# Performance work log

Measured on AMD Instinct MI355X. Metric: run time of the kernel, lower is better.

The kernel has to match this reference:

```python
import jax, jax.numpy as jnp
import numpy as np

D_MODEL = 1024
D_STATE = 16
EXPAND = 2
D_HEAD = 64
D_CONV = 4
FFN = 2816
NORMALIZE_BC = True
D_INNER = EXPAND * D_MODEL          # 2048
N_HEADS = D_INNER // D_HEAD         # 32
EPS = 1e-6


def _rmsnorm(x, w):
    v = jnp.mean(x * x, axis=-1, keepdims=True)
    return x * jax.lax.rsqrt(v + EPS) * w


def _mixer(x, in_proj_w, conv_w, conv_b, A_log, dt_bias, D, out_proj_w):
    b, l, _ = x.shape
    zxbcdt = x @ in_proj_w.T  # (b, l, 2*D_INNER + 2*D_STATE + N_HEADS)
    z, xBC, dt_raw = jnp.split(zxbcdt, [D_INNER, 2 * D_INNER + 2 * D_STATE], axis=-1)
    # causal depthwise conv over (u, B, C) channels
    xp = jnp.pad(xBC, ((0, 0), (D_CONV - 1, 0), (0, 0)))
    y = conv_b + sum(xp[:, k:k + l, :] * conv_w[:, k] for k in range(D_CONV))
    xBC = jax.nn.silu(y)
    u, Bm, Cm = jnp.split(xBC, [D_INNER, D_INNER + D_STATE], axis=-1)
    if NORMALIZE_BC:
        Bm = Bm / (jnp.linalg.norm(Bm, axis=-1, keepdims=True) + EPS)
        Cm = Cm / (jnp.linalg.norm(Cm, axis=-1, keepdims=True) + EPS)
    dt = jax.nn.softplus(dt_raw + dt_bias)          # (b, l, h)
    A = jnp.exp(A_log)                              # (h, n) oscillator frequencies >= 0
    u = u.reshape(b, l, N_HEADS, D_HEAD)

    # LinOSS implicit (IM) discretization of z' = -A y + B u ; y' = z
    #   S  = 1/(1 + dt^2 A)
    #   w_k = S*(w_{k-1} - dt*A*y_{k-1} + dt*B u_k)
    #   y_k = y_{k-1} + dt*w_k ;  out_k = C y_k + D u_k
    def step(carry, inp):
        w, ys = carry                               # each (b, h, dh, n)
        dt_t, B_t, C_t, u_t = inp                   # (b,h),(b,n),(b,n),(b,h,dh)
        S = 1.0 / (1.0 + (dt_t[:, :, None] ** 2) * A[None])   # (b,h,n)
        Sb = S[:, :, None, :]
        dtb = dt_t[:, :, None, None]
        Ab = A[None, :, None, :]
        Bu = B_t[:, None, None, :] * u_t[..., None]            # (b,h,dh,n)
        w = Sb * (w - dtb * Ab * ys + dtb * Bu)
        ys = ys + dtb * w
        o = jnp.einsum('bhdn,bn->bhd', ys, C_t)
        return (w, ys), o

    init = (jnp.zeros((b, N_HEADS, D_HEAD, D_STATE), x.dtype),
            jnp.zeros((b, N_HEADS, D_HEAD, D_STATE), x.dtype))
    xs = (dt.transpose(1, 0, 2), Bm.transpose(1, 0, 2),
          Cm.transpose(1, 0, 2), u.transpose(1, 0, 2, 3))
    _, ys = jax.lax.scan(step, init, xs)            # (l, b, h, dh)
    ys = ys.transpose(1, 0, 2, 3) + D[None, None, :, None] * u
    out = ys.reshape(b, l, D_INNER) * jax.nn.silu(z)
    return out @ out_proj_w.T


def setup_inputs() -> dict:
    key = jax.random.key(0)
    ks = jax.random.split(key, 12)
    B, L = 4, 2048
    proj_dim = 2 * D_INNER + 2 * D_STATE + N_HEADS
    conv_ch = D_INNER + 2 * D_STATE
    s = lambda k, shape, sc: jax.random.normal(k, shape, jnp.float32) * sc
    return {
        "x": s(ks[0], (B, L, D_MODEL), 1.0),
        "norm1_w": jnp.ones((D_MODEL,), jnp.float32),
        "in_proj_w": s(ks[1], (proj_dim, D_MODEL), D_MODEL ** -0.5),
        "conv_w": s(ks[2], (conv_ch, D_CONV), 0.3),
        "conv_b": jnp.zeros((conv_ch,), jnp.float32),
        "A_log": s(ks[3], (N_HEADS, D_STATE), 0.5),
        "dt_bias": s(ks[4], (N_HEADS,), 0.5),
        "D": s(ks[5], (N_HEADS,), 1.0),
        "out_proj_w": s(ks[6], (D_MODEL, D_INNER), D_INNER ** -0.5),
        "norm2_w": jnp.ones((D_MODEL,), jnp.float32),
        "gate_w": s(ks[7], (FFN, D_MODEL), D_MODEL ** -0.5),
        "up_w": s(ks[8], (FFN, D_MODEL), D_MODEL ** -0.5),
        "down_w": s(ks[9], (D_MODEL, FFN), FFN ** -0.5),
    }


def reference(x, norm1_w, in_proj_w, conv_w, conv_b, A_log, dt_bias, D,
              out_proj_w, norm2_w, gate_w, up_w, down_w):
    h = x + _mixer(_rmsnorm(x, norm1_w), in_proj_w, conv_w, conv_b,
                   A_log, dt_bias, D, out_proj_w)
    hn = _rmsnorm(h, norm2_w)
    ffn = (jax.nn.silu(hn @ gate_w.T) * (hn @ up_w.T)) @ down_w.T
    return h + ffn
```

## Files before the change

### kernel.cpp

```cpp
#include <hip/hip_runtime.h>
#include <hip/hip_bf16.h>

#define D_MODEL   1024
#define D_STATE   16
#define D_HEAD    64
#define D_CONV    4
#define FFN_DIM   2816
#define D_INNER   2048
#define N_HEADS   32
#define BATCH     4
#define SEQ       2048
#define ROWS      (BATCH*SEQ)
#define PROJ_DIM  4160
#define PROJ_PAD  4352
#define CONV_CH   2080
#define CH        128
#define NCH       (SEQ/CH)
#define GU_N      5632

typedef __bf16 bf16x8 __attribute__((ext_vector_type(8)));
typedef float  f32x4  __attribute__((ext_vector_type(4)));
typedef float  f32x2  __attribute__((ext_vector_type(2)));

__device__ __forceinline__ float siluf(float x) { return x / (1.0f + __expf(-x)); }

#define SBAR() do { asm volatile("" ::: "memory"); __builtin_amdgcn_s_barrier(); asm volatile("" ::: "memory"); } while (0)
#define LGKM0() asm volatile("s_waitcnt lgkmcnt(0)" ::: "memory")
#define VMCNT4() asm volatile("s_waitcnt vmcnt(4)" ::: "memory")
#define VMCNT2() asm volatile("s_waitcnt vmcnt(2)" ::: "memory")
#define VMCNT0() asm volatile("s_waitcnt vmcnt(0)" ::: "memory")

__global__ void cvt_k(const float* __restrict__ src, __hip_bfloat16* __restrict__ dst, int n) {
  int i = blockIdx.x * blockDim.x + threadIdx.x;
  if (i < n) dst[i] = __float2bfloat16(src[i]);
}

__global__ void cvt_pad_k(const float* __restrict__ src, __hip_bfloat16* __restrict__ dst) {
  int i = blockIdx.x * blockDim.x + threadIdx.x;
  if (i >= PROJ_PAD * D_MODEL) return;
  int row = i >> 10;
  dst[i] = (row < PROJ_DIM) ? __float2bfloat16(src[i]) : __float2bfloat16(0.0f);
}

__global__ void cvt_gu_k(const float* __restrict__ wg, const float* __restrict__ wu,
                         __hip_bfloat16* __restrict__ dst) {
  int i = blockIdx.x * blockDim.x + threadIdx.x;
  if (i >= GU_N * D_MODEL) return;
  int r = i >> 10, c = i & 1023;
  int tile = r >> 8, rr = r & 255;
  const float* src = (rr < 128)
      ? wg + (size_t)(tile * 128 + rr) * D_MODEL + c
      : wu + (size_t)(tile * 128 + (rr - 128)) * D_MODEL + c;
  dst[i] = __float2bfloat16(*src);
}

__global__ __launch_bounds__(256) void rmsnorm_k(const float* __restrict__ x,
                                                 const float* __restrict__ w,
                                                 __hip_bfloat16* __restrict__ out,
                                                 float* __restrict__ outf) {
  int row = blockIdx.x;
  int t = threadIdx.x;
  const float* xr = x + (size_t)row * D_MODEL;
  float4 v = ((const float4*)xr)[t];
  float ss = v.x*v.x + v.y*v.y + v.z*v.z + v.w*v.w;
  #pragma unroll
  for (int o = 32; o > 0; o >>= 1) ss += __shfl_xor(ss, o);
  __shared__ float red[4];
  if ((t & 63) == 0) red[t >> 6] = ss;
  __syncthreads();
  ss = red[0] + red[1] + red[2] + red[3];
  float scale = rsqrtf(ss * (1.0f / D_MODEL) + 1e-6f);
  float4 wv = ((const float4*)w)[t];
  float4 r;
  r.x = v.x * scale * wv.x; r.y = v.y * scale * wv.y;
  r.z = v.z * scale * wv.z; r.w = v.w * scale * wv.w;
  __hip_bfloat16* orow = out + (size_t)row * D_MODEL + t * 4;
  orow[0] = __float2bfloat16(r.x);
  orow[1] = __float2bfloat16(r.y);
  orow[2] = __float2bfloat16(r.z);
  orow[3] = __float2bfloat16(r.w);
  if (outf) ((float4*)(outf + (size_t)row * D_MODEL))[t] = r;
}

__global__ __launch_bounds__(256) void dtproj_k(const float* __restrict__ xn,
                                                const float* __restrict__ wi,
                                                const float* __restrict__ dtb,
                                                float* __restrict__ dtT) {
  const int r0 = blockIdx.x * 4;
  const int t  = threadIdx.x;
  const int hh  = t >> 3;
  const int seg = t & 7;

  __shared__ float xs[4][D_MODEL];
  #pragma unroll
  for (int i = 0; i < 4; ++i)
    ((float4*)&xs[i][0])[t] = ((const float4*)(xn + (size_t)(r0 + i) * D_MODEL))[t];
  __syncthreads();

  const float4* w4 = (const float4*)(wi + (size_t)(2 * D_INNER + 2 * D_STATE + hh) * D_MODEL) + seg * 32;
  const float4* x0 = (const float4*)&xs[0][0] + seg * 32;
  const float4* x1 = (const float4*)&xs[1][0] + seg * 32;
  const float4* x2 = (const float4*)&xs[2][0] + seg * 32;
  const float4* x3 = (const float4*)&xs[3][0] + seg * 32;
  float a0 = 0.f, a1 = 0.f, a2 = 0.f, a3 = 0.f;
  #pragma unroll 8
  for (int k = 0; k < 32; ++k) {
    float4 wv = w4[k];
    float4 v0 = x0[k], v1 = x1[k], v2 = x2[k], v3 = x3[k];
    a0 = fmaf(wv.x, v0.x, fmaf(wv.y, v0.y, fmaf(wv.z, v0.z, fmaf(wv.w, v0.w, a0))));
    a1 = fmaf(wv.x, v1.x, fmaf(wv.y, v1.y, fmaf(wv.z, v1.z, fmaf(wv.w, v1.w, a1))));
    a2 = fmaf(wv.x, v2.x, fmaf(wv.y, v2.y, fmaf(wv.z, v2.z, fmaf(wv.w, v2.w, a2))));
    a3 = fmaf(wv.x, v3.x, fmaf(wv.y, v3.y, fmaf(wv.z, v3.z, fmaf(wv.w, v3.w, a3))));
  }
  #pragma unroll
  for (int m = 1; m < 8; m <<= 1) {
    a0 += __shfl_xor(a0, m);
    a1 += __shfl_xor(a1, m);
    a2 += __shfl_xor(a2, m);
    a3 += __shfl_xor(a3, m);
  }
  if (seg == 0) {
    float bias = dtb[hh];
    float v[4] = {a0, a1, a2, a3};
    #pragma unroll
    for (int i = 0; i < 4; ++i) {
      float xv = v[i] + bias;
      dtT[(size_t)hh * ROWS + r0 + i] = (xv > 20.f) ? xv : log1pf(__expf(xv));
    }
  }
}

template<int EPI>
__global__ __launch_bounds__(512, 2) void gemm8(
    const __hip_bfloat16* __restrict__ A,
    const __hip_bfloat16* __restrict__ Bw,
    float* __restrict__ Cf,
    __hip_bfloat16* __restrict__ Cb,
    const float* __restrict__ add_src,
    int M, int N, int K)
{
  extern __shared__ char lds[];
  const int nwg = (M >> 8) * (N >> 8);
  int bid = blockIdx.x;
  bid = (bid & 7) * (nwg >> 3) + (bid >> 3);
  const int ntn = N >> 8;
  const int bm = (bid / ntn) << 8;
  const int bn = (bid % ntn) << 8;

  const int tid  = threadIdx.x;
  const int wid  = tid >> 6;
  const int lane = tid & 63;
  const int wm = wid >> 2;
  const int wn = wid & 3;
  const int r16 = lane & 15;
  const int kg  = lane >> 4;

  const int rb = ((r16 << 6) + (kg << 4)) ^ ((r16 & 8) << 2);

  const int s_sub = tid >> 6;
  const int s_w   = (tid & 63) << 4;
  const int s_wp  = s_w ^ ((((s_w) >> 9) & 1) << 5);
  const int s_row = ((s_sub >> 1) << 4) + (s_wp >> 6);
  const int s_col = ((s_sub & 1) << 5) + ((s_wp >> 1) & 31);

  auto stage = [&](int buf, int mat, int half, int c, int kt) {
    const __hip_bfloat16* src = (mat == 0)
        ? A  + (size_t)(bm + half * 128 + c * 64 + s_row) * K + kt * 64 + s_col
        : Bw + (size_t)(bn + half * 128 + c * 64 + s_row) * K + kt * 64 + s_col;
    char* dst = lds + buf * 65536 + mat * 32768 + half * 16384 + c * 8192 + tid * 16;
    __builtin_amdgcn_global_load_lds((const __attribute__((address_space(1))) unsigned int*)src,
                                     (__attribute__((address_space(3))) unsigned int*)dst,
                                     16, 0, 0);
  };

  f32x4 acc[8][4] = {};
  bf16x8 af[4][2], bfr[4][2];

  const int NT = K >> 6;
  stage(0,0,0,0,0); stage(0,0,0,1,0); stage(0,0,1,0,0); stage(0,0,1,1,0);
  stage(0,1,0,0,0); stage(0,1,0,1,0); stage(0,1,1,0,0); stage(0,1,1,1,0);
  __syncthreads();

  for (int kt = 0; kt < NT; ++kt) {
    const int buf = kt & 1, nbuf = buf ^ 1;
    const bool st = (kt + 1 < NT);
    const char* Ab = lds + buf * 65536 + wm * 16384;
    const char* Bb = lds + buf * 65536 + 32768 + (wn >> 1) * 16384 + (wn & 1) * 8192;

    #pragma unroll
    for (int mi2 = 0; mi2 < 4; ++mi2)
      #pragma unroll
      for (int kk = 0; kk < 2; ++kk)
        af[mi2][kk] = *(const bf16x8*)(Ab + (mi2 * 2 + kk) * 1024 + rb);
    #pragma unroll
    for (int ni = 0; ni < 2; ++ni)
      #pragma unroll
      for (int kk = 0; kk < 2; ++kk)
        bfr[ni][kk] = *(const bf16x8*)(Bb + (ni * 2 + kk) * 1024 + rb);
    if (st) { stage(nbuf,1,0,0,kt+1); stage(nbuf,1,0,1,kt+1); }
    SBAR(); LGKM0();
    __builtin_amdgcn_s_setprio(1);
    #pragma unroll
    for (int mi2 = 0; mi2 < 4; ++mi2)
      #pragma unroll
      for (int ni = 0; ni < 2; ++ni)
        #pragma unroll
        for (int kk = 0; kk < 2; ++kk)
          acc[mi2][ni] = __builtin_amdgcn_mfma_f32_16x16x32_bf16(af[mi2][kk], bfr[ni][kk], acc[mi2][ni], 0, 0, 0);
    __builtin_amdgcn_s_setprio(0);
    SBAR();

    #pragma unroll
    for (int ni = 2; ni < 4; ++ni)
      #pragma unroll
      for (int kk = 0; kk < 2; ++kk)
        bfr[ni][kk] = *(const bf16x8*)(Bb + (ni * 2 + kk) * 1024 + rb);
    if (st) { stage(nbuf,1,1,0,kt+1); stage(nbuf,1,1,1,kt+1); }
    SBAR(); LGKM0();
    __builtin_amdgcn_s_setprio(1);
    #pragma unroll
    for (int mi2 = 0; mi2 < 4; ++mi2)
      #pragma unroll
      for (int ni = 2; ni < 4; ++ni)
        #pragma unroll
        for (int kk = 0; kk < 2; ++kk)
          acc[mi2][ni] = __builtin_amdgcn_mfma_f32_16x16x32_bf16(af[mi2][kk], bfr[ni][kk], acc[mi2][ni], 0, 0, 0);
    __builtin_amdgcn_s_setprio(0);
    if (st) { VMCNT4(); } else { VMCNT0(); }
    SBAR();

    #pragma unroll
    for (int mi2 = 0; mi2 < 4; ++mi2)
      #pragma unroll
      for (int kk = 0; kk < 2; ++kk)
        af[mi2][kk] = *(const bf16x8*)(Ab + ((4 + mi2) * 2 + kk) * 1024 + rb);
    if (st) { stage(nbuf,0,0,0,kt+1); stage(nbuf,0,1,0,kt+1); }
    SBAR(); LGKM0();
    __builtin_amdgcn_s_setprio(1);
    #pragma unroll
    for (int mi2 = 0; mi2 < 4; ++mi2)
      #pragma unroll
      for (int ni = 0; ni < 2; ++ni)
        #pragma unroll
        for (int kk = 0; kk < 2; ++kk)
          acc[4 + mi2][ni] = __builtin_amdgcn_mfma_f32_16x16x32_bf16(af[mi2][kk], bfr[ni][kk], acc[4 + mi2][ni], 0, 0, 0);
    __builtin_amdgcn_s_setprio(0);
    SBAR();

    if (st) { stage(nbuf,0,0,1,kt+1); stage(nbuf,0,1,1,kt+1); }
    SBAR(); LGKM0();
    __builtin_amdgcn_s_setprio(1);
    #pragma unroll
    for (int mi2 = 0; mi2 < 4; ++mi2)
      #pragma unroll
      for (int ni = 2; ni < 4; ++ni)
        #pragma unroll
        for (int kk = 0; kk < 2; ++kk)
          acc[4 + mi2][ni] = __builtin_amdgcn_mfma_f32_16x16x32_bf16(af[mi2][kk], bfr[ni][kk], acc[4 + mi2][ni], 0, 0, 0);
    __builtin_amdgcn_s_setprio(0);
    VMCNT2();
    SBAR();
  }

  if constexpr (EPI == 4) {
    float* xch = (float*)lds;
    __syncthreads();
    if (wn < 2) {
      #pragma unroll
      for (int mi = 0; mi < 8; ++mi)
        #pragma unroll
        for (int ni = 0; ni < 4; ++ni)
          #pragma unroll
          for (int j = 0; j < 4; ++j) {
            int row = mi * 16 + kg * 4 + j;
            int col = wn * 64 + ni * 16 + r16;
            int cc = col ^ (((row >> 2) & 1) << 4);
            xch[wm * 16384 + row * 128 + cc] = siluf(acc[mi][ni][j]);
          }
    }
    __syncthreads();
    if (wn >= 2) {
      #pragma unroll
      for (int mi = 0; mi < 8; ++mi)
        #pragma unroll
        for (int ni = 0; ni < 4; ++ni)
          #pragma unroll
          for (int j = 0; j < 4; ++j) {
            int row = mi * 16 + kg * 4 + j;
            int col = (wn - 2) * 64 + ni * 16 + r16;
            int cc = col ^ (((row >> 2) & 1) << 4);
            float g = xch[wm * 16384 + row * 128 + cc];
            int r = bm + wm * 128 + row;
            int tc = (bn >> 1) + col;
            Cb[(size_t)r * FFN_DIM + tc] = __float2bfloat16(g * acc[mi][ni][j]);
          }
    }
  } else {
    #pragma unroll
    for (int mi = 0; mi < 8; ++mi) {
      #pragma unroll
      for (int ni = 0; ni < 4; ++ni) {
        #pragma unroll
        for (int j = 0; j < 4; ++j) {
          int r = bm + wm * 128 + mi * 16 + kg * 4 + j;
          int c = bn + wn * 64 + ni * 16 + r16;
          size_t idx = (size_t)r * N + c;
          float v = acc[mi][ni][j];
          if constexpr (EPI == 0) {
            Cf[idx] = v;
          } else if constexpr (EPI == 1) {
            Cf[idx] = v + add_src[idx];
          }
        }
      }
    }
  }
}

template<int EPI>
__global__ __launch_bounds__(512, 2) void gemm8B(
    const __hip_bfloat16* __restrict__ A,
    const __hip_bfloat16* __restrict__ Bw,
    float* __restrict__ Cf,
    __hip_bfloat16* __restrict__ Cb,
    const float* __restrict__ add_src,
    int M, int N, int K)
{
  extern __shared__ char lds[];
  const int nwg = (M >> 8) * (N >> 7);
  int bid = blockIdx.x;
  bid = (bid & 7) * (nwg >> 3) + (bid >> 3);
  const int ntn = N >> 7;
  const int bm = (bid / ntn) << 8;
  const int bn = (bid % ntn) << 7;

  const int tid  = threadIdx.x;
  const int wid  = tid >> 6;
  const int lane = tid & 63;
  const int wm = wid >> 2;
  const int wn = wid & 3;
  const int r16 = lane & 15;
  const int kg  = lane >> 4;

  const int rb = ((r16 << 6) + (kg << 4)) ^ ((r16 & 8) << 2);

  const int s_sub = tid >> 6;
  const int s_w   = (tid & 63) << 4;
  const int s_wp  = s_w ^ ((((s_w) >> 9) & 1) << 5);
  const int s_row = ((s_sub >> 1) << 4) + (s_wp >> 6);
  const int s_col = ((s_sub & 1) << 5) + ((s_wp >> 1) & 31);

  auto stageA = [&](int buf, int half, int c, int kt) {
    const __hip_bfloat16* src = A + (size_t)(bm + half * 128 + c * 64 + s_row) * K + kt * 64 + s_col;
    char* dst = lds + buf * 65536 + half * 16384 + c * 8192 + tid * 16;
    __builtin_amdgcn_global_load_lds((const __attribute__((address_space(1))) unsigned int*)src,
                                     (__attribute__((address_space(3))) unsigned int*)dst,
                                     16, 0, 0);
  };
  auto stageB = [&](int buf, int c, int kt) {
    const __hip_bfloat16* src = Bw + (size_t)(bn + c * 64 + s_row) * K + kt * 64 + s_col;
    char* dst = lds + buf * 65536 + 32768 + c * 8192 + tid * 16;
    __builtin_amdgcn_global_load_lds((const __attribute__((address_space(1))) unsigned int*)src,
                                     (__attribute__((address_space(3))) unsigned int*)dst,
                                     16, 0, 0);
  };

  f32x4 acc[8][2] = {};
  bf16x8 af[4][2], bfr[2][2];

  const int NT = K >> 6;
  stageB(0,0,0); stageB(0,1,0);
  stageA(0,0,0,0); stageA(0,1,0,0); stageA(0,0,1,0); stageA(0,1,1,0);
  __syncthreads();

  for (int kt = 0; kt < NT; ++kt) {
    const int buf = kt & 1, nbuf = buf ^ 1;
    const bool st = (kt + 1 < NT);
    const char* Ab = lds + buf * 65536 + wm * 16384;
    const char* Bb = lds + buf * 65536 + 32768 + (wn >> 1) * 8192 + (wn & 1) * 4096;

    #pragma unroll
    for (int mi2 = 0; mi2 < 4; ++mi2)
      #pragma unroll
      for (int kk = 0; kk < 2; ++kk)
        af[mi2][kk] = *(const bf16x8*)(Ab + (mi2 * 2 + kk) * 1024 + rb);
    #pragma unroll
    for (int ni = 0; ni < 2; ++ni)
      #pragma unroll
      for (int kk = 0; kk < 2; ++kk)
        bfr[ni][kk] = *(const bf16x8*)(Bb + (ni * 2 + kk) * 1024 + rb);
    if (st) { stageB(nbuf,0,kt+1); stageB(nbuf,1,kt+1); stageA(nbuf,0,0,kt+1); stageA(nbuf,1,0,kt+1); }
    SBAR(); LGKM0();
    __builtin_amdgcn_s_setprio(1);
    #pragma unroll
    for (int mi2 = 0; mi2 < 4; ++mi2)
      #pragma unroll
      for (int ni = 0; ni < 2; ++ni)
        #pragma unroll
        for (int kk = 0; kk < 2; ++kk)
          acc[mi2][ni] = __builtin_amdgcn_mfma_f32_16x16x32_bf16(af[mi2][kk], bfr[ni][kk], acc[mi2][ni], 0, 0, 0);
    __builtin_amdgcn_s_setprio(0);
    if (st) { VMCNT4(); } else { VMCNT0(); }
    SBAR();

    #pragma unroll
    for (int mi2 = 0; mi2 < 4; ++mi2)
      #pragma unroll
      for (int kk = 0; kk < 2; ++kk)
        af[mi2][kk] = *(const bf16x8*)(Ab + ((4 + mi2) * 2 + kk) * 1024 + rb);
    if (st) { stageA(nbuf,0,1,kt+1); stageA(nbuf,1,1,kt+1); }
    SBAR(); LGKM0();
    __builtin_amdgcn_s_setprio(1);
    #pragma unroll
    for (int mi2 = 0; mi2 < 4; ++mi2)
      #pragma unroll
      for (int ni = 0; ni < 2; ++ni)
        #pragma unroll
        for (int kk = 0; kk < 2; ++kk)
          acc[4 + mi2][ni] = __builtin_amdgcn_mfma_f32_16x16x32_bf16(af[mi2][kk], bfr[ni][kk], acc[4 + mi2][ni], 0, 0, 0);
    __builtin_amdgcn_s_setprio(0);
    VMCNT2();
    SBAR();
  }

  #pragma unroll
  for (int mi = 0; mi < 8; ++mi) {
    #pragma unroll
    for (int ni = 0; ni < 2; ++ni) {
      #pragma unroll
      for (int j = 0; j < 4; ++j) {
        int r = bm + wm * 128 + mi * 16 + kg * 4 + j;
        int c = bn + wn * 32 + ni * 16 + r16;
        size_t idx = (size_t)r * N + c;
        float v = acc[mi][ni][j];
        if constexpr (EPI == 0) {
          Cf[idx] = v;
        } else if constexpr (EPI == 1) {
          Cf[idx] = v + add_src[idx];
        }
      }
    }
  }
}

__global__ __launch_bounds__(256) void duconv_k(const float* __restrict__ zx,
                                                const float* __restrict__ cw,
                                                const float* __restrict__ cb,
                                                __hip_bfloat16* __restrict__ u_po) {
  int idx = blockIdx.x * 256 + threadIdx.x;
  int q = idx & 511;
  int r = idx >> 9;
  int d0 = q << 2;
  int l = r & (SEQ - 1);
  float4 cb4 = ((const float4*)cb)[q];
  float tw[4][4];
  #pragma unroll
  for (int i = 0; i < 4; ++i) {
    float4 t = ((const float4*)cw)[d0 + i];
    tw[i][0] = t.x; tw[i][1] = t.y; tw[i][2] = t.z; tw[i][3] = t.w;
  }
  float a[4] = {cb4.x, cb4.y, cb4.z, cb4.w};
  #pragma unroll
  for (int k = 0; k < 4; ++k) {
    if (l - 3 + k >= 0) {
      float4 xv = *(const float4*)(zx + (size_t)(r - 3 + k) * PROJ_PAD + D_INNER + d0);
      a[0] = fmaf(xv.x, tw[0][k], a[0]);
      a[1] = fmaf(xv.y, tw[1][k], a[1]);
      a[2] = fmaf(xv.z, tw[2][k], a[2]);
      a[3] = fmaf(xv.w, tw[3][k], a[3]);
    }
  }
  union { ushort4 u4; __hip_bfloat16 b[4]; } pk;
  #pragma unroll
  for (int i = 0; i < 4; ++i) pk.b[i] = __float2bfloat16(siluf(a[i]));
  *(ushort4*)(u_po + (size_t)r * D_INNER + d0) = pk.u4;
}

__global__ __launch_bounds__(256) void bcdt_k(const float* __restrict__ zx,
                                              const float* __restrict__ cw,
                                              const float* __restrict__ cb,
                                              float* __restrict__ bc) {
  int t = threadIdx.x;
  int r = blockIdx.x * 8 + (t >> 5);
  int ch = t & 31;
  int l = r & (SEQ - 1);
  int c = D_INNER + ch;
  float acc = cb[c];
  #pragma unroll
  for (int k = 0; k < 4; ++k) {
    int lp = l - 3 + k;
    if (lp >= 0)
      acc = fmaf(zx[(size_t)(r - 3 + k) * PROJ_PAD + 2 * D_INNER + ch], cw[c * 4 + k], acc);
  }
  acc = siluf(acc);
  float ss = acc * acc;
  ss += __shfl_xor(ss, 1);
  ss += __shfl_xor(ss, 2);
  ss += __shfl_xor(ss, 4);
  ss += __shfl_xor(ss, 8);
  bc[r * 32 + ch] = acc / (sqrtf(ss) + 1e-6f);
}

__global__ __launch_bounds__(256) void pk_k(const float* __restrict__ dtT,
                                            const float* __restrict__ A_log,
                                            float* __restrict__ Pm) {
  int bh = blockIdx.x;
  int h = bh & 31;
  int t = threadIdx.x;
  int ch = t >> 4, n = t & 15;
  float a = __expf(A_log[h * 16 + n]);
  const float* dtp = dtT + (size_t)h * ROWS + (size_t)(bh >> 5) * SEQ + ch * CH;
  float p00 = 1.f, p01 = 0.f, p10 = 0.f, p11 = 1.f;
  for (int l = 0; l < CH; ++l) {
    float dt = dtp[l];
    float s  = 1.0f / fmaf(dt * dt, a, 1.0f);
    float m00 = s;
    float m01 = -dt * a * s;
    float m10 = dt * s;
    float m11 = fmaf(-dt * a, m10, 1.0f);
    float q00 = fmaf(m00, p00, m01 * p10);
    float q01 = fmaf(m00, p01, m01 * p11);
    float q10 = fmaf(m10, p00, m11 * p10);
    float q11 = fmaf(m10, p01, m11 * p11);
    p00 = q00; p01 = q01; p10 = q10; p11 = q11;
  }
  float4 v = {p00, p01, p10, p11};
  *(float4*)&Pm[(((size_t)bh * NCH + ch) * 16 + n) * 4] = v;
}

__global__ __launch_bounds__(256) void prop_k(const float* __restrict__ Pm,
                                              const float* __restrict__ pend,
                                              float* __restrict__ sinit) {
  int gid = blockIdx.x * 256 + threadIdx.x;
  int n  = gid & 15;
  int d  = (gid >> 4) & 63;
  int bh = gid >> 10;
  float s0 = 0.f, s1 = 0.f;
  for (int c = 0; c < NCH; ++c) {
    size_t i2 = (((size_t)bh * NCH + c) * 64 + d) * 16 + n;
    *(float2*)&sinit[i2 * 2] = make_float2(s0, s1);
    float4 P  = *(const float4*)&Pm[(((size_t)bh * NCH + c) * 16 + n) * 4];
    float2 pe = *(const float2*)&pend[i2 * 2];
    float t0 = fmaf(P.x, s0, fmaf(P.y, s1, pe.x));
    float t1 = fmaf(P.z, s0, fmaf(P.w, s1, pe.y));
    s0 = t0; s1 = t1;
  }
}

#define T_TILE 16
#define TPC (CH / T_TILE)
template<int PHASE>
__global__ __launch_bounds__(128) void scan_k(
    const float* __restrict__ zx, const float* __restrict__ bcb,
    const float* __restrict__ dtT, const float* __restrict__ A_log,
    const float* __restrict__ Dp, float* __restrict__ states,
    __hip_bfloat16* u_po)
{
  const int blk  = blockIdx.x;
  const int half = blk & 1;
  const int ch   = (blk >> 1) & 15;
  const int h    = (blk >> 5) & 31;
  const int b    = blk >> 10;
  const int bh   = b * 32 + h;
  const int tid  = threadIdx.x;
  const int wv   = tid >> 6;
  const int lane = tid & 63;
  const int d16  = lane & 15;
  const int ng   = lane >> 4;
  const int n0   = ng * 4;
  const int dwv  = wv * 16 + d16;
  const int dl   = half * 32 + dwv;
  const int dbase = h * 64 + half * 32;
  const size_t rowbase = (size_t)b * SEQ + (size_t)ch * CH;

  __shared__ __hip_bfloat16 dut[2][T_TILE][32];
  __shared__ float Btl[2][T_TILE][16];
  __shared__ float Ctl[PHASE == 3 ? 2 : 1][T_TILE][16];
  __shared__ float zt [PHASE == 3 ? 2 : 1][T_TILE][32];
  __shared__ float st [2][T_TILE][16];
  __shared__ float dtt[2][T_TILE];
  __shared__ float aexp[16];
  __shared__ float opart[PHASE == 3 ? T_TILE : 1][32][4];

  if (tid < 16) aexp[tid] = __expf(A_log[h * 16 + tid]);

  f32x2 A2[2];
  #pragma unroll
  for (int k = 0; k < 2; ++k) {
    A2[k][0] = __expf(A_log[h * 16 + n0 + 2 * k]);
    A2[k][1] = __expf(A_log[h * 16 + n0 + 2 * k + 1]);
  }
  const float Dh = Dp[h];

  auto stage = [&](int tile, int buf) {
    const size_t r0 = rowbase + (size_t)tile * T_TILE;
    if constexpr (PHASE == 3) {
      {
        int row = wv * 8 + (lane >> 3);
        const float* g = zx + (r0 + row) * PROJ_PAD + dbase + (lane & 7) * 4;
        float* l_ = &zt[buf][0][0] + wv * 256 + lane * 4;
        __builtin_amdgcn_global_load_lds((const __attribute__((address_space(1))) unsigned int*)g,
                                         (__attribute__((address_space(3))) unsigned int*)l_, 16, 0, 0);
      }
      if (wv == 0) {
        const __hip_bfloat16* g = u_po + (r0 + (lane >> 2)) * D_INNER + dbase + (lane & 3) * 8;
        __hip_bfloat16* l_ = &dut[buf][0][0] + lane * 8;
        __builtin_amdgcn_global_load_lds((const __attribute__((address_space(1))) unsigned int*)g,
                                         (__attribute__((address_space(3))) unsigned int*)l_, 16, 0, 0);
      } else {
        const float* gB = bcb + (r0 + (lane >> 2)) * 32 + (lane & 3) * 4;
        float* lB = &Btl[buf][0][0] + lane * 4;
        __builtin_amdgcn_global_load_lds((const __attribute__((address_space(1))) unsigned int*)gB,
                                         (__attribute__((address_space(3))) unsigned int*)lB, 16, 0, 0);
        const float* gC = bcb + (r0 + (lane >> 2)) * 32 + 16 + (lane & 3) * 4;
        float* lC = &Ctl[buf][0][0] + lane * 4;
        __builtin_amdgcn_global_load_lds((const __attribute__((address_space(1))) unsigned int*)gC,
                                         (__attribute__((address_space(3))) unsigned int*)lC, 16, 0, 0);
      }
    } else {
      if (wv == 0) {
        const __hip_bfloat16* g = u_po + (r0 + (lane >> 2)) * D_INNER + dbase + (lane & 3) * 8;
        __hip_bfloat16* l_ = &dut[buf][0][0] + lane * 8;
        __builtin_amdgcn_global_load_lds((const __attribute__((address_space(1))) unsigned int*)g,
                                         (__attribute__((address_space(3))) unsigned int*)l_, 16, 0, 0);
      } else {
        const float* gB = bcb + (r0 + (lane >> 2)) * 32 + (lane & 3) * 4;
        float* lB = &Btl[buf][0][0] + lane * 4;
        __builtin_amdgcn_global_load_lds((const __attribute__((address_space(1))) unsigned int*)gB,
                                         (__attribute__((address_space(3))) unsigned int*)lB, 16, 0, 0);
      }
    }
  };

  auto sprep = [&](int buf, float dtn) {
    #pragma unroll
    for (int i = 0; i < 2; ++i) {
      int idx = tid + 128 * i;
      int row = idx >> 4, n = idx & 15;
      float dv = __shfl(dtn, row);
      float a  = aexp[n];
      st[buf][row][n] = 1.0f / fmaf(dv * dv, a, 1.0f);
    }
  };

  stage(0, 0);
  float dtn = 0.f;
  if (lane < 16) dtn = dtT[(size_t)h * ROWS + rowbase + lane];
  __syncthreads();
  if (tid < 16) dtt[0][tid] = dtn;
  sprep(0, dtn);
  __syncthreads();

  f32x2 w2[2], ys2[2];
  if constexpr (PHASE == 1) {
    #pragma unroll
    for (int k = 0; k < 2; ++k) { w2[k] = (f32x2){0.f, 0.f}; ys2[k] = (f32x2){0.f, 0.f}; }
  } else {
    #pragma unroll
    for (int k = 0; k < 2; ++k)
      #pragma unroll
      for (int j = 0; j < 2; ++j) {
        size_t i2 = (((size_t)bh * NCH + ch) * 64 + dl) * 16 + (n0 + 2 * k + j);
        float2 s = *(const float2*)&states[i2 * 2];
        w2[k][j] = s.x; ys2[k][j] = s.y;
      }
  }
  int cur = 0;

  for (int t = 0; t < TPC; ++t) {
    if (t + 1 < TPC) {
      stage(t + 1, cur ^ 1);
      if (lane < 16) dtn = dtT[(size_t)h * ROWS + rowbase + (size_t)(t + 1) * T_TILE + lane];
    }
    #pragma unroll 4
    for (int l = 0; l < T_TILE; ++l) {
      float uv  = __bfloat162float(dut[cur][l][dwv]);
      float dtv = dtt[cur][l];
      f32x4 Sv4 = *(const f32x4*)&st [cur][l][n0];
      f32x4 Bv4 = *(const f32x4*)&Btl[cur][l][n0];
      float du = dtv * uv;
      f32x2 S2[2] = { {Sv4[0], Sv4[1]}, {Sv4[2], Sv4[3]} };
      f32x2 B2[2] = { {Bv4[0], Bv4[1]}, {Bv4[2], Bv4[3]} };
      if constexpr (PHASE == 3) {
        f32x4 Cv4 = *(const f32x4*)&Ctl[cur][l][n0];
        f32x2 C2[2] = { {Cv4[0], Cv4[1]}, {Cv4[2], Cv4[3]} };
        f32x2 o2 = {0.f, 0.f};
        #pragma unroll
        for (int k = 0; k < 2; ++k) {
          f32x2 dtA = dtv * A2[k];
          f32x2 tmp = w2[k] - dtA * ys2[k];
          tmp = tmp + du * B2[k];
          w2[k] = S2[k] * tmp;
          ys2[k] = ys2[k] + dtv * w2[k];
          o2 = o2 + ys2[k] * C2[k];
        }
        float o = o2[0] + o2[1];
        float ofin = (ng == 0) ? fmaf(Dh, uv, o) : o;
        opart[l][dwv][ng] = ofin;
      } else {
        #pragma unroll
        for (int k = 0; k < 2; ++k) {
          f32x2 dtA = dtv * A2[k];
          f32x2 tmp = w2[k] - dtA * ys2[k];
          tmp = tmp + du * B2[k];
          w2[k] = S2[k] * tmp;
          ys2[k] = ys2[k] + dtv * w2[k];
        }
      }
    }
    if constexpr (PHASE == 3) {
      #pragma unroll
      for (int i = 0; i < 4; ++i) {
        int l  = (lane >> 4) + 4 * i;
        int dd = wv * 16 + d16;
        f32x4 op = *(const f32x4*)&opart[l][dd][0];
        float zv = zt[cur][l][dd];
        float yv = (op[0] + op[1]) + (op[2] + op[3]);
        u_po[(rowbase + (size_t)t * T_TILE + l) * D_INNER + dbase + dd] =
            __float2bfloat16(yv * siluf(zv));
      }
    }
    __syncthreads();
    if (t + 1 < TPC) {
      if (tid < 16) dtt[cur ^ 1][tid] = dtn;
      sprep(cur ^ 1, dtn);
      __syncthreads();
    }
    cur ^= 1;
  }

  if constexpr (PHASE == 1) {
    #pragma unroll
    for (int k = 0; k < 2; ++k)
      #pragma unroll
      for (int j = 0; j < 2; ++j) {
        size_t i2 = (((size_t)bh * NCH + ch) * 64 + dl) * 16 + (n0 + 2 * k + j);
        *(float2*)&states[i2 * 2] = make_float2(w2[k][j], ys2[k][j]);
      }
  }
}

extern "C" void kernel_launch(void* const* d_in, const int* in_sizes, int n_in,
                              void* d_out, int out_size, void* d_ws, size_t ws_size,
                              hipStream_t stream) {
  const float* x     = (const float*)d_in[0];
  const float* n1w   = (const float*)d_in[1];
  const float* wi    = (const float*)d_in[2];
  const float* cw    = (const float*)d_in[3];
  const float* cb    = (const float*)d_in[4];
  const float* A_log = (const float*)d_in[5];
  const float* dtb   = (const float*)d_in[6];
  const float* Dp    = (const float*)d_in[7];
  const float* wo    = (const float*)d_in[8];
  const float* n2w   = (const float*)d_in[9];
  const float* wg    = (const float*)d_in[10];
  const float* wu    = (const float*)d_in[11];
  const float* wd    = (const float*)d_in[12];
  float* out = (float*)d_out;

  char* p = (char*)d_ws;
  auto take = [&](size_t b) { char* q = p; p += (b + 255) & ~(size_t)255; return q; };
  __hip_bfloat16* wbi  = (__hip_bfloat16*)take((size_t)PROJ_PAD * D_MODEL * 2);
  __hip_bfloat16* wbo  = (__hip_bfloat16*)take((size_t)D_MODEL * D_INNER * 2);
  __hip_bfloat16* wgu  = (__hip_bfloat16*)take((size_t)GU_N * D_MODEL * 2);
  __hip_bfloat16* wbd  = (__hip_bfloat16*)take((size_t)D_MODEL * FFN_DIM * 2);
  __hip_bfloat16* h0b  = (__hip_bfloat16*)take((size_t)ROWS * D_MODEL * 2);
  float*          zx   = (float*)take((size_t)ROWS * PROJ_PAD * 4);
  float*          bcb  = (float*)take((size_t)ROWS * 32 * 4);
  float*          dtT  = (float*)take((size_t)ROWS * 32 * 4);
  __hip_bfloat16* po   = (__hip_bfloat16*)take((size_t)ROWS * D_INNER * 2);
  float*          pend = (float*)take((size_t)128 * NCH * 64 * 16 * 2 * 4);
  float*          sini = (float*)take((size_t)128 * NCH * 64 * 16 * 2 * 4);
  float*          Pm   = (float*)take((size_t)128 * NCH * 16 * 4 * 4);
  float*          h0f  = (float*)zx;
  float*          h    = (float*)zx;
  __hip_bfloat16* gact = (__hip_bfloat16*)((char*)zx + 33554432);

  hipFuncSetAttribute(reinterpret_cast<const void*>(&gemm8<0>),  hipFuncAttributeMaxDynamicSharedMemorySize, 131072);
  hipFuncSetAttribute(reinterpret_cast<const void*>(&gemm8<4>),  hipFuncAttributeMaxDynamicSharedMemorySize, 131072);
  hipFuncSetAttribute(reinterpret_cast<const void*>(&gemm8B<1>), hipFuncAttributeMaxDynamicSharedMemorySize, 131072);

  cvt_pad_k<<<(PROJ_PAD * D_MODEL + 255) / 256, 256, 0, stream>>>(wi, wbi);
  cvt_k<<<(D_MODEL * D_INNER + 255) / 256, 256, 0, stream>>>(wo, wbo, D_MODEL * D_INNER);
  cvt_gu_k<<<(GU_N * D_MODEL + 255) / 256, 256, 0, stream>>>(wg, wu, wgu);
  cvt_k<<<(FFN_DIM * D_MODEL + 255) / 256, 256, 0, stream>>>(wd, wbd, FFN_DIM * D_MODEL);

  rmsnorm_k<<<ROWS, 256, 0, stream>>>(x, n1w, h0b, h0f);
  dtproj_k<<<ROWS / 4, 256, 0, stream>>>(h0f, wi, dtb, dtT);
  gemm8<0><<<(ROWS / 256) * (PROJ_PAD / 256), 512, 131072, stream>>>(h0b, wbi, zx, nullptr, nullptr,
                                                                     ROWS, PROJ_PAD, D_MODEL);
  duconv_k<<<ROWS * 512 / 256, 256, 0, stream>>>(zx, cw, cb, po);
  bcdt_k<<<ROWS / 8, 256, 0, stream>>>(zx, cw, cb, bcb);
  pk_k<<<BATCH * N_HEADS, 256, 0, stream>>>(dtT, A_log, Pm);
  scan_k<1><<<BATCH * N_HEADS * NCH * 2, 128, 0, stream>>>(zx, bcb, dtT, A_log, Dp, pend, po);
  prop_k<<<BATCH * N_HEADS * 64 * 16 / 256, 256, 0, stream>>>(Pm, pend, sini);
  scan_k<3><<<BATCH * N_HEADS * NCH * 2, 128, 0, stream>>>(zx, bcb, dtT, A_log, Dp, sini, po);
  gemm8B<1><<<(ROWS / 256) * (D_MODEL / 128), 512, 131072, stream>>>(po, wbo, h, nullptr, x,
                                                                     ROWS, D_MODEL, D_INNER);
  rmsnorm_k<<<ROWS, 256, 0, stream>>>(h, n2w, h0b, nullptr);
  gemm8<4><<<(ROWS / 256) * (GU_N / 256), 512, 131072, stream>>>(h0b, wgu, nullptr, gact, nullptr,
                                                                 ROWS, GU_N, D_MODEL);
  gemm8B<1><<<(ROWS / 256) * (D_MODEL / 128), 512, 131072, stream>>>(gact, wbd, out, nullptr, h,
                                                                     ROWS, D_MODEL, FFN_DIM);
}
```

Baseline: 648.8 us.

## Shrink in-projection GEMM to 4096 columns with bf16 output, move B/C to vector kernel

The in-projection GEMM now covers only the z and x columns (4096 instead of a padded 4352) and writes bf16 instead of fp32. The 32 B/C projection rows are computed in fp32 by the small vector-projection kernel alongside dt. Conv and scan kernels read the bf16 buffer, which roughly halves the traffic of the large intermediate and drops the padded tile column. The cost is extra work in the vector-projection kernel and reduced precision for z and x.

```diff
diff --git a/kernel.cpp b/kernel.cpp
--- a/kernel.cpp
+++ b/kernel.cpp
@@ -12,8 +12,7 @@
 #define SEQ       2048
 #define ROWS      (BATCH*SEQ)
 #define PROJ_DIM  4160
-#define PROJ_PAD  4352
-#define CONV_CH   2080
+#define ZX_N      4096
 #define CH        128
 #define NCH       (SEQ/CH)
 #define GU_N      5632
@@ -33,13 +32,6 @@
 __global__ void cvt_k(const float* __restrict__ src, __hip_bfloat16* __restrict__ dst, int n) {
   int i = blockIdx.x * blockDim.x + threadIdx.x;
   if (i < n) dst[i] = __float2bfloat16(src[i]);
-}
-
-__global__ void cvt_pad_k(const float* __restrict__ src, __hip_bfloat16* __restrict__ dst) {
-  int i = blockIdx.x * blockDim.x + threadIdx.x;
-  if (i >= PROJ_PAD * D_MODEL) return;
-  int row = i >> 10;
-  dst[i] = (row < PROJ_DIM) ? __float2bfloat16(src[i]) : __float2bfloat16(0.0f);
 }
 
 __global__ void cvt_gu_k(const float* __restrict__ wg, const float* __restrict__ wu,
@@ -82,14 +74,15 @@
   if (outf) ((float4*)(outf + (size_t)row * D_MODEL))[t] = r;
 }
 
-__global__ __launch_bounds__(256) void dtproj_k(const float* __restrict__ xn,
-                                                const float* __restrict__ wi,
-                                                const float* __restrict__ dtb,
-                                                float* __restrict__ dtT) {
+__global__ __launch_bounds__(256) void vecproj_k(const float* __restrict__ xn,
+                                                 const float* __restrict__ wi,
+                                                 const float* __restrict__ dtb,
+                                                 float* __restrict__ dtT,
+                                                 float* __restrict__ bcraw) {
   const int r0 = blockIdx.x * 4;
   const int t  = threadIdx.x;
-  const int hh  = t >> 3;
-  const int seg = t & 7;
+  const int o   = t >> 2;
+  const int seg = t & 3;
 
   __shared__ float xs[4][D_MODEL];
   #pragma unroll
@@ -97,14 +90,15 @@
     ((float4*)&xs[i][0])[t] = ((const float4*)(xn + (size_t)(r0 + i) * D_MODEL))[t];
   __syncthreads();
 
-  const float4* w4 = (const float4*)(wi + (size_t)(2 * D_INNER + 2 * D_STATE + hh) * D_MODEL) + seg * 32;
-  const float4* x0 = (const float4*)&xs[0][0] + seg * 32;
-  const float4* x1 = (const float4*)&xs[1][0] + seg * 32;
-  const float4* x2 = (const float4*)&xs[2][0] + seg * 32;
-  const float4* x3 = (const float4*)&xs[3][0] + seg * 32;
+  const int wrow = (o < 32) ? (2 * D_INNER + o) : (2 * D_INNER + 2 * D_STATE + (o - 32));
+  const float4* w4 = (const float4*)(wi + (size_t)wrow * D_MODEL) + seg * 64;
+  const float4* x0 = (const float4*)&xs[0][0] + seg * 64;
+  const float4* x1 = (const float4*)&xs[1][0] + seg * 64;
+  const float4* x2 = (const float4*)&xs[2][0] + seg * 64;
+  const float4* x3 = (const float4*)&xs[3][0] + seg * 64;
   float a0 = 0.f, a1 = 0.f, a2 = 0.f, a3 = 0.f;
   #pragma unroll 8
-  for (int k = 0; k < 32; ++k) {
+  for (int k = 0; k < 64; ++k) {
     float4 wv = w4[k];
     float4 v0 = x0[k], v1 = x1[k], v2 = x2[k], v3 = x3[k];
     a0 = fmaf(wv.x, v0.x, fmaf(wv.y, v0.y, fmaf(wv.z, v0.z, fmaf(wv.w, v0.w, a0))));
@@ -113,19 +107,25 @@
     a3 = fmaf(wv.x, v3.x, fmaf(wv.y, v3.y, fmaf(wv.z, v3.z, fmaf(wv.w, v3.w, a3))));
   }
   #pragma unroll
-  for (int m = 1; m < 8; m <<= 1) {
+  for (int m = 1; m < 4; m <<= 1) {
     a0 += __shfl_xor(a0, m);
     a1 += __shfl_xor(a1, m);
     a2 += __shfl_xor(a2, m);
     a3 += __shfl_xor(a3, m);
   }
   if (seg == 0) {
-    float bias = dtb[hh];
     float v[4] = {a0, a1, a2, a3};
-    #pragma unroll
-    for (int i = 0; i < 4; ++i) {
-      float xv = v[i] + bias;
-      dtT[(size_t)hh * ROWS + r0 + i] = (xv > 20.f) ? xv : log1pf(__expf(xv));
+    if (o < 32) {
+      #pragma unroll
+      for (int i = 0; i < 4; ++i) bcraw[(size_t)(r0 + i) * 32 + o] = v[i];
+    } else {
+      int hh = o - 32;
+      float bias = dtb[hh];
+      #pragma unroll
+      for (int i = 0; i < 4; ++i) {
+        float xv = v[i] + bias;
+        dtT[(size_t)hh * ROWS + r0 + i] = (xv > 20.f) ? xv : log1pf(__expf(xv));
+      }
     }
   }
 }
@@ -310,6 +310,8 @@
             Cf[idx] = v;
           } else if constexpr (EPI == 1) {
             Cf[idx] = v + add_src[idx];
+          } else if constexpr (EPI == 5) {
+            Cb[idx] = __float2bfloat16(v);
           }
         }
       }
@@ -443,7 +445,7 @@
   }
 }
 
-__global__ __launch_bounds__(256) void duconv_k(const float* __restrict__ zx,
+__global__ __launch_bounds__(256) void duconv_k(const __hip_bfloat16* __restrict__ zxb,
                                                 const float* __restrict__ cw,
                                                 const float* __restrict__ cb,
                                                 __hip_bfloat16* __restrict__ u_po) {
@@ -463,11 +465,12 @@
   #pragma unroll
   for (int k = 0; k < 4; ++k) {
     if (l - 3 + k >= 0) {
-      float4 xv = *(const float4*)(zx + (size_t)(r - 3 + k) * PROJ_PAD + D_INNER + d0);
-      a[0] = fmaf(xv.x, tw[0][k], a[0]);
-      a[1] = fmaf(xv.y, tw[1][k], a[1]);
-      a[2] = fmaf(xv.z, tw[2][k], a[2]);
-      a[3] = fmaf(xv.w, tw[3][k], a[3]);
+      union { ushort4 u4; __hip_bfloat16 b[4]; } R;
+      R.u4 = *(const ushort4*)(zxb + (size_t)(r - 3 + k) * ZX_N + D_INNER + d0);
+      a[0] = fmaf(__bfloat162float(R.b[0]), tw[0][k], a[0]);
+      a[1] = fmaf(__bfloat162float(R.b[1]), tw[1][k], a[1]);
+      a[2] = fmaf(__bfloat162float(R.b[2]), tw[2][k], a[2]);
+      a[3] = fmaf(__bfloat162float(R.b[3]), tw[3][k], a[3]);
     }
   }
   union { ushort4 u4; __hip_bfloat16 b[4]; } pk;
@@ -476,7 +479,7 @@
   *(ushort4*)(u_po + (size_t)r * D_INNER + d0) = pk.u4;
 }
 
-__global__ __launch_bounds__(256) void bcdt_k(const float* __restrict__ zx,
+__global__ __launch_bounds__(256) void bcdt_k(const float* __restrict__ bcraw,
                                               const float* __restrict__ cw,
                                               const float* __restrict__ cb,
                                               float* __restrict__ bc) {
@@ -490,7 +493,7 @@
   for (int k = 0; k < 4; ++k) {
     int lp = l - 3 + k;
     if (lp >= 0)
-      acc = fmaf(zx[(size_t)(r - 3 + k) * PROJ_PAD + 2 * D_INNER + ch], cw[c * 4 + k], acc);
+      acc = fmaf(bcraw[(size_t)(r - 3 + k) * 32 + ch], cw[c * 4 + k], acc);
   }
   acc = siluf(acc);
   float ss = acc * acc;
@@ -551,7 +554,7 @@
 #define TPC (CH / T_TILE)
 template<int PHASE>
 __global__ __launch_bounds__(128) void scan_k(
-    const float* __restrict__ zx, const float* __restrict__ bcb,
+    const __hip_bfloat16* __restrict__ zxb, const float* __restrict__ bcb,
     const float* __restrict__ dtT, const float* __restrict__ A_log,
     const float* __restrict__ Dp, float* __restrict__ states,
     __hip_bfloat16* u_po)
@@ -576,7 +579,7 @@
   __shared__ __hip_bfloat16 dut[2][T_TILE][32];
   __shared__ float Btl[2][T_TILE][16];
   __shared__ float Ctl[PHASE == 3 ? 2 : 1][T_TILE][16];
-  __shared__ float zt [PHASE == 3 ? 2 : 1][T_TILE][32];
+  __shared__ __hip_bfloat16 zt [PHASE == 3 ? 2 : 1][T_TILE][32];
   __shared__ float st [2][T_TILE][16];
   __shared__ float dtt[2][T_TILE];
   __shared__ float aexp[16];
@@ -595,19 +598,16 @@
   auto stage = [&](int tile, int buf) {
     const size_t r0 = rowbase + (size_t)tile * T_TILE;
     if constexpr (PHASE == 3) {
-      {
-        int row = wv * 8 + (lane >> 3);
-        const float* g = zx + (r0 + row) * PROJ_PAD + dbase + (lane & 7) * 4;
-        float* l_ = &zt[buf][0][0] + wv * 256 + lane * 4;
-        __builtin_amdgcn_global_load_lds((const __attribute__((address_space(1))) unsigned int*)g,
-                                         (__attribute__((address_space(3))) unsigned int*)l_, 16, 0, 0);
-      }
       if (wv == 0) {
         const __hip_bfloat16* g = u_po + (r0 + (lane >> 2)) * D_INNER + dbase + (lane & 3) * 8;
         __hip_bfloat16* l_ = &dut[buf][0][0] + lane * 8;
         __builtin_amdgcn_global_load_lds((const __attribute__((address_space(1))) unsigned int*)g,
                                          (__attribute__((address_space(3))) unsigned int*)l_, 16, 0, 0);
       } else {
+        const __hip_bfloat16* gz = zxb + (r0 + (lane >> 2)) * ZX_N + dbase + (lane & 3) * 8;
+        __hip_bfloat16* lz = &zt[buf][0][0] + lane * 8;
+        __builtin_amdgcn_global_load_lds((const __attribute__((address_space(1))) unsigned int*)gz,
+                                         (__attribute__((address_space(3))) unsigned int*)lz, 16, 0, 0);
         const float* gB = bcb + (r0 + (lane >> 2)) * 32 + (lane & 3) * 4;
         float* lB = &Btl[buf][0][0] + lane * 4;
         __builtin_amdgcn_global_load_lds((const __attribute__((address_space(1))) unsigned int*)gB,
@@ -714,7 +714,7 @@
         int l  = (lane >> 4) + 4 * i;
         int dd = wv * 16 + d16;
         f32x4 op = *(const f32x4*)&opart[l][dd][0];
-        float zv = zt[cur][l][dd];
+        float zv = __bfloat162float(zt[cur][l][dd]);
         float yv = (op[0] + op[1]) + (op[2] + op[3]);
         u_po[(rowbase + (size_t)t * T_TILE + l) * D_INNER + dbase + dd] =
             __float2bfloat16(yv * siluf(zv));
@@ -760,41 +760,43 @@
 
   char* p = (char*)d_ws;
   auto take = [&](size_t b) { char* q = p; p += (b + 255) & ~(size_t)255; return q; };
-  __hip_bfloat16* wbi  = (__hip_bfloat16*)take((size_t)PROJ_PAD * D_MODEL * 2);
+  __hip_bfloat16* wbi  = (__hip_bfloat16*)take((size_t)ZX_N * D_MODEL * 2);
   __hip_bfloat16* wbo  = (__hip_bfloat16*)take((size_t)D_MODEL * D_INNER * 2);
   __hip_bfloat16* wgu  = (__hip_bfloat16*)take((size_t)GU_N * D_MODEL * 2);
   __hip_bfloat16* wbd  = (__hip_bfloat16*)take((size_t)D_MODEL * FFN_DIM * 2);
   __hip_bfloat16* h0b  = (__hip_bfloat16*)take((size_t)ROWS * D_MODEL * 2);
-  float*          zx   = (float*)take((size_t)ROWS * PROJ_PAD * 4);
+  char*           region = take((size_t)84 * 1024 * 1024);
   float*          bcb  = (float*)take((size_t)ROWS * 32 * 4);
+  float*          bcraw= (float*)take((size_t)ROWS * 32 * 4);
   float*          dtT  = (float*)take((size_t)ROWS * 32 * 4);
   __hip_bfloat16* po   = (__hip_bfloat16*)take((size_t)ROWS * D_INNER * 2);
   float*          pend = (float*)take((size_t)128 * NCH * 64 * 16 * 2 * 4);
   float*          sini = (float*)take((size_t)128 * NCH * 64 * 16 * 2 * 4);
   float*          Pm   = (float*)take((size_t)128 * NCH * 16 * 4 * 4);
-  float*          h0f  = (float*)zx;
-  float*          h    = (float*)zx;
-  __hip_bfloat16* gact = (__hip_bfloat16*)((char*)zx + 33554432);
-
-  hipFuncSetAttribute(reinterpret_cast<const void*>(&gemm8<0>),  hipFuncAttributeMaxDynamicSharedMemorySize, 131072);
+  float*          h0f  = (float*)region;
+  __hip_bfloat16* zxb  = (__hip_bfloat16*)region;
+  float*          h    = (float*)region;
+  __hip_bfloat16* gact = (__hip_bfloat16*)(region + 33554432);
+
+  hipFuncSetAttribute(reinterpret_cast<const void*>(&gemm8<5>),  hipFuncAttributeMaxDynamicSharedMemorySize, 131072);
   hipFuncSetAttribute(reinterpret_cast<const void*>(&gemm8<4>),  hipFuncAttributeMaxDynamicSharedMemorySize, 131072);
   hipFuncSetAttribute(reinterpret_cast<const void*>(&gemm8B<1>), hipFuncAttributeMaxDynamicSharedMemorySize, 131072);
 
-  cvt_pad_k<<<(PROJ_PAD * D_MODEL + 255) / 256, 256, 0, stream>>>(wi, wbi);
+  cvt_k<<<(ZX_N * D_MODEL + 255) / 256, 256, 0, stream>>>(wi, wbi, ZX_N * D_MODEL);
   cvt_k<<<(D_MODEL * D_INNER + 255) / 256, 256, 0, stream>>>(wo, wbo, D_MODEL * D_INNER);
   cvt_gu_k<<<(GU_N * D_MODEL + 255) / 256, 256, 0, stream>>>(wg, wu, wgu);
   cvt_k<<<(FFN_DIM * D_MODEL + 255) / 256, 256, 0, stream>>>(wd, wbd, FFN_DIM * D_MODEL);
 
   rmsnorm_k<<<ROWS, 256, 0, stream>>>(x, n1w, h0b, h0f);
-  dtproj_k<<<ROWS / 4, 256, 0, stream>>>(h0f, wi, dtb, dtT);
-  gemm8<0><<<(ROWS / 256) * (PROJ_PAD / 256), 512, 131072, stream>>>(h0b, wbi, zx, nullptr, nullptr,
-                                                                     ROWS, PROJ_PAD, D_MODEL);
-  duconv_k<<<ROWS * 512 / 256, 256, 0, stream>>>(zx, cw, cb, po);
-  bcdt_k<<<ROWS / 8, 256, 0, stream>>>(zx, cw, cb, bcb);
+  vecproj_k<<<ROWS / 4, 256, 0, stream>>>(h0f, wi, dtb, dtT, bcraw);
+  gemm8<5><<<(ROWS / 256) * (ZX_N / 256), 512, 131072, stream>>>(h0b, wbi, nullptr, zxb, nullptr,
+                                                                 ROWS, ZX_N, D_MODEL);
+  duconv_k<<<ROWS * 512 / 256, 256, 0, stream>>>(zxb, cw, cb, po);
+  bcdt_k<<<ROWS / 8, 256, 0, stream>>>(bcraw, cw, cb, bcb);
   pk_k<<<BATCH * N_HEADS, 256, 0, stream>>>(dtT, A_log, Pm);
-  scan_k<1><<<BATCH * N_HEADS * NCH * 2, 128, 0, stream>>>(zx, bcb, dtT, A_log, Dp, pend, po);
+  scan_k<1><<<BATCH * N_HEADS * NCH * 2, 128, 0, stream>>>(zxb, bcb, dtT, A_log, Dp, pend, po);
   prop_k<<<BATCH * N_HEADS * 64 * 16 / 256, 256, 0, stream>>>(Pm, pend, sini);
-  scan_k<3><<<BATCH * N_HEADS * NCH * 2, 128, 0, stream>>>(zx, bcb, dtT, A_log, Dp, sini, po);
+  scan_k<3><<<BATCH * N_HEADS * NCH * 2, 128, 0, stream>>>(zxb, bcb, dtT, A_log, Dp, sini, po);
   gemm8B<1><<<(ROWS / 256) * (D_MODEL / 128), 512, 131072, stream>>>(po, wbo, h, nullptr, x,
                                                                      ROWS, D_MODEL, D_INNER);
   rmsnorm_k<<<ROWS, 256, 0, stream>>>(h, n2w, h0b, nullptr);
```

New measurement: 606.8 us. -6.5%, faster.
